# Performance work log

Measured on AMD Instinct MI355X. Metric: run time of the kernel, lower is better.

Reference implementation:

```python
import jax, jax.numpy as jnp
import numpy as np

ARITY = 2
DEPTH = 9          # max_depth: full tree has levels 0..DEPTH
H = 512            # hidden_size
V = 512            # vocab_size
B = 64             # batch
S = 64             # source length


def _preorder_perm(arity, depth):
    # map pre-order position -> flat level-order index
    offs = np.cumsum([0] + [arity ** d for d in range(depth + 1)])
    perm = []
    def rec(d, pos):
        perm.append(int(offs[d] + pos))
        if d < depth:
            for c in range(arity):
                rec(d + 1, pos * arity + c)
    rec(0, 0)
    return np.asarray(perm, dtype=np.int32)

PERM = jnp.asarray(_preorder_perm(ARITY, DEPTH))


def setup_inputs() -> dict:
    key = jax.random.key(0)
    ks = jax.random.split(key, 12)
    s = 0.05
    return {
        "root_hiddens": jax.random.normal(ks[0], (B, H), jnp.float32),
        "ann_emb": jax.random.normal(ks[1], (B, H), jnp.float32),
        "encoder_outputs": jax.random.normal(ks[2], (S, B, H), jnp.float32),
        "source_mask": jnp.ones((B, S), dtype=bool),
        # GRUCell params per child: input_size = 2H (attention concat)
        "w_ih": jax.random.normal(ks[3], (ARITY, 3 * H, 2 * H), jnp.float32) * s,
        "w_hh": jax.random.normal(ks[4], (ARITY, 3 * H, H), jnp.float32) * s,
        "b_ih": jax.random.normal(ks[5], (ARITY, 3 * H), jnp.float32) * s,
        "b_hh": jax.random.normal(ks[6], (ARITY, 3 * H), jnp.float32) * s,
        # hidden2vocab: Linear(H,2H) -> Sigmoid -> Linear(2H,V)
        "W1": jax.random.normal(ks[7], (2 * H, H), jnp.float32) * s,
        "b1": jax.random.normal(ks[8], (2 * H,), jnp.float32) * s,
        "W2": jax.random.normal(ks[9], (V, 2 * H), jnp.float32) * s,
        "b2": jax.random.normal(ks[10], (V,), jnp.float32) * s,
    }


def _gru(x, h, wih, whh, bih, bhh):
    # x: [B,n,2H], h: [B,n,H]; PyTorch GRUCell semantics
    gi = jnp.einsum('bni,gi->bng', x, wih) + bih
    gh = jnp.einsum('bnh,gh->bng', h, whh) + bhh
    i_r, i_z, i_n = jnp.split(gi, 3, axis=-1)
    h_r, h_z, h_n = jnp.split(gh, 3, axis=-1)
    r = jax.nn.sigmoid(i_r + h_r)
    z = jax.nn.sigmoid(i_z + h_z)
    n = jnp.tanh(i_n + r * h_n)
    return (1.0 - z) * n + z * h


def _forward(root_hiddens, ann_emb, encoder_outputs, source_mask,
             w_ih, w_hh, b_ih, b_hh, W1, b1, W2, b2):
    b = root_hiddens.shape[0]
    enc = encoder_outputs.transpose(1, 0, 2)        # [B,S,H]
    h = root_hiddens[:, None, :]                    # [B,1,H]
    prods = []
    for d in range(DEPTH + 1):
        # hidden2vocab at every node of this level
        hid = jax.nn.sigmoid(jnp.einsum('bnh,kh->bnk', h, W1) + b1)
        prods.append(jnp.einsum('bnk,vk->bnv', hid, W2) + b2)
        if d < DEPTH:
            # dot-product attention per node over source positions
            scores = jnp.einsum('bnh,bsh->bns', h, enc)
            scores = jnp.where(source_mask[:, None, :], scores, -1e9)
            a = jax.nn.softmax(scores, axis=-1)
            weighted = jnp.einsum('bns,bsh->bnh', a, enc)
            n = h.shape[1]
            x = jnp.concatenate(
                [jnp.broadcast_to(ann_emb[:, None, :], (b, n, H)), weighted],
                axis=-1)                             # [B,n,2H]
            children = [_gru(x, h, w_ih[c], w_hh[c], b_ih[c], b_hh[c])
                        for c in range(ARITY)]
            h = jnp.stack(children, axis=2).reshape(b, n * ARITY, H)
    out = jnp.concatenate(prods, axis=1)            # [B,N,V] level-order
    out = out[:, PERM, :]                           # pre-order, as torch yields
    return out.transpose(1, 0, 2)                   # [N,B,V] like pad_sequence


def reference(root_hiddens, ann_emb, encoder_outputs, source_mask,
              w_ih, w_hh, b_ih, b_hh, W1, b1, W2, b2):
    return _forward(root_hiddens, ann_emb, encoder_outputs, source_mask,
                    w_ih, w_hh, b_ih, b_hh, W1, b1, W2, b2)
```

## Files before the change

### kernel.cpp

```cpp
#include <hip/hip_runtime.h>


#define BATCH 64
#define HDIM  512

typedef float  floatx4 __attribute__((ext_vector_type(4)));
typedef float  f32x16  __attribute__((ext_vector_type(16)));
typedef short  short8  __attribute__((ext_vector_type(8)));

__device__ __forceinline__ float bf2f(unsigned short u) {
  union { unsigned int i; float f; } v; v.i = ((unsigned int)u) << 16; return v.f;
}
__device__ __forceinline__ unsigned short f2bf(float f) {
  union { float f; unsigned int i; } v; v.f = f;
  unsigned int x = v.i;
  return (unsigned short)((x + 0x7fffu + ((x >> 16) & 1u)) >> 16);
}
__device__ __forceinline__ float sigm(float x) { return 1.f / (1.f + __expf(-x)); }

__device__ __forceinline__ int preorder_idx(int d, int node) {
  int p = 0;
  for (int i = 1; i <= d; ++i) {
    int bit = (node >> (d - i)) & 1;
    p += 1 + bit * ((1 << (10 - i)) - 1);
  }
  return p;
}

__device__ __forceinline__ void gload_lds16(const void* g, void* l) {
  __builtin_amdgcn_global_load_lds(
      (const __attribute__((address_space(1))) unsigned int*)g,
      (__attribute__((address_space(3))) unsigned int*)l, 16, 0, 0);
}

__device__ __forceinline__ void stage_f32(unsigned short* ldst, const float* src) {
  float4 v0 = *(const float4*)src;
  float4 v1 = *(const float4*)(src + 4);
  union { unsigned short s[8]; float4 v; } u;
  u.s[0]=f2bf(v0.x); u.s[1]=f2bf(v0.y); u.s[2]=f2bf(v0.z); u.s[3]=f2bf(v0.w);
  u.s[4]=f2bf(v1.x); u.s[5]=f2bf(v1.y); u.s[6]=f2bf(v1.z); u.s[7]=f2bf(v1.w);
  *(float4*)ldst = u.v;
}

__device__ __forceinline__ void stage_split(unsigned short* dh, unsigned short* dl,
                                            const float* src) {
  float4 v0 = *(const float4*)src;
  float4 v1 = *(const float4*)(src + 4);
  float v[8] = {v0.x, v0.y, v0.z, v0.w, v1.x, v1.y, v1.z, v1.w};
  union { unsigned short s[8]; float4 q; } H, L;
  #pragma unroll
  for (int i = 0; i < 8; ++i) {
    unsigned short hb = f2bf(v[i]);
    H.s[i] = hb;
    L.s[i] = f2bf(v[i] - bf2f(hb));
  }
  *(float4*)dh = H.q;
  *(float4*)dl = L.q;
}

__global__ __launch_bounds__(256) void k_root(const float* __restrict__ root,
                                              float* __restrict__ h0,
                                              unsigned short* __restrict__ bh,
                                              unsigned short* __restrict__ bl) {
  int i = blockIdx.x * 256 + threadIdx.x;
  float v = root[i];
  h0[i] = v;
  int row = i >> 9, k = i & 511;
  int mt = row >> 5, r = row & 31, ktg = k >> 4, oct = (k >> 3) & 1, e = k & 7;
  size_t fo = ((size_t)(mt * 32 + ktg) * 64 + oct * 32 + r) * 8 + e;
  unsigned short hb = f2bf(v);
  bh[fo] = hb;
  bl[fo] = f2bf(v - bf2f(hb));
}

__global__ __launch_bounds__(256) void k_prep_wih(const float* __restrict__ wih,
                                                  unsigned short* __restrict__ dh,
                                                  unsigned short* __restrict__ dl) {
  int idx = blockIdx.x * 256 + threadIdx.x;
  int jr  = idx & 31;
  int oct = (idx >> 5) & 1;
  int ktg = (idx >> 6) & 31;
  int jt  = (idx >> 11) & 15;
  int cg  = idx >> 15;
  int c = cg / 3, g = cg % 3;
  int j = jt * 32 + jr, k = ktg * 16 + oct * 8;
  const float* src = wih + ((size_t)c * 1536 + g * 512 + j) * 1024 + 512 + k;
  float v[8];
  *(float4*)&v[0] = *(const float4*)src;
  *(float4*)&v[4] = *(const float4*)(src + 4);
  union { unsigned short s[8]; float4 q; } H, L;
  #pragma unroll
  for (int i = 0; i < 8; ++i) {
    unsigned short hb = f2bf(v[i]); H.s[i] = hb; L.s[i] = f2bf(v[i] - bf2f(hb));
  }
  *(float4*)(dh + (size_t)idx * 8) = H.q;
  *(float4*)(dl + (size_t)idx * 8) = L.q;
}

__global__ __launch_bounds__(256) void k_prep_whh(const float* __restrict__ whh,
                                                  unsigned short* __restrict__ dh,
                                                  unsigned short* __restrict__ dl) {
  int idx = blockIdx.x * 256 + threadIdx.x;
  int jr  = idx & 31;
  int oct = (idx >> 5) & 1;
  int ktg = (idx >> 6) & 31;
  int jt  = (idx >> 11) & 15;
  int cg  = idx >> 15;
  int c = cg / 3, g = cg % 3;
  int j = jt * 32 + jr, k = ktg * 16 + oct * 8;
  const float* src = whh + ((size_t)c * 1536 + g * 512 + j) * 512 + k;
  float v[8];
  *(float4*)&v[0] = *(const float4*)src;
  *(float4*)&v[4] = *(const float4*)(src + 4);
  union { unsigned short s[8]; float4 q; } H, L;
  #pragma unroll
  for (int i = 0; i < 8; ++i) {
    unsigned short hb = f2bf(v[i]); H.s[i] = hb; L.s[i] = f2bf(v[i] - bf2f(hb));
  }
  *(float4*)(dh + (size_t)idx * 8) = H.q;
  *(float4*)(dl + (size_t)idx * 8) = L.q;
}

__global__ __launch_bounds__(256) void k_prep_encB(const float* __restrict__ enc,
                                                   unsigned short* __restrict__ dh,
                                                   unsigned short* __restrict__ dl) {
  int idx = blockIdx.x * 256 + threadIdx.x;
  int jr  = idx & 31;
  int oct = (idx >> 5) & 1;
  int ktg = (idx >> 6) & 31;
  int jt  = (idx >> 11) & 1;
  int b   = idx >> 12;
  int s = jt * 32 + jr, k = ktg * 16 + oct * 8;
  const float* src = enc + ((size_t)s * 64 + b) * 512 + k;
  float v[8];
  *(float4*)&v[0] = *(const float4*)src;
  *(float4*)&v[4] = *(const float4*)(src + 4);
  union { unsigned short s_[8]; float4 q; } H, L;
  #pragma unroll
  for (int i = 0; i < 8; ++i) {
    unsigned short hb = f2bf(v[i]); H.s_[i] = hb; L.s_[i] = f2bf(v[i] - bf2f(hb));
  }
  *(float4*)(dh + (size_t)idx * 8) = H.q;
  *(float4*)(dl + (size_t)idx * 8) = L.q;
}

__global__ __launch_bounds__(256) void k_prep_encT(const float* __restrict__ enc,
                                                   unsigned short* __restrict__ dh,
                                                   unsigned short* __restrict__ dl) {
  int idx = blockIdx.x * 256 + threadIdx.x;
  int jr  = idx & 31;
  int oct = (idx >> 5) & 1;
  int ktg = (idx >> 6) & 3;
  int jt  = (idx >> 8) & 15;
  int b   = idx >> 12;
  int hcol = jt * 32 + jr, s0 = ktg * 16 + oct * 8;
  float v[8];
  #pragma unroll
  for (int e = 0; e < 8; ++e)
    v[e] = enc[((size_t)(s0 + e) * 64 + b) * 512 + hcol];
  union { unsigned short s_[8]; float4 q; } H, L;
  #pragma unroll
  for (int i = 0; i < 8; ++i) {
    unsigned short hb = f2bf(v[i]); H.s_[i] = hb; L.s_[i] = f2bf(v[i] - bf2f(hb));
  }
  *(float4*)(dh + (size_t)idx * 8) = H.q;
  *(float4*)(dl + (size_t)idx * 8) = L.q;
}

__global__ __launch_bounds__(256) void k_prep_bf(const float* __restrict__ src,
                                                 unsigned short* __restrict__ db) {
  size_t i = ((size_t)blockIdx.x * 256 + threadIdx.x) * 8;
  stage_f32(db + i, src + i);
}

__global__ __launch_bounds__(256) void k_giann(const float* __restrict__ ann,
                                               const float* __restrict__ wih,
                                               float* __restrict__ giann) {
  __shared__ __align__(16) unsigned short lah[64*40], lal[64*40];
  __shared__ __align__(16) unsigned short lwh[64*40], lwl[64*40];
  int t = threadIdx.x, lane = t & 63, wv = t >> 6;
  int jbase = blockIdx.y * 64, c = blockIdx.z;
  const float* wih_c = wih + (size_t)c * 1536 * 1024;
  floatx4 acc[4];
  #pragma unroll
  for (int i = 0; i < 4; ++i) acc[i] = (floatx4)(0.f);
  int srow = t >> 2, skk = (t & 3) * 8;
  for (int k0 = 0; k0 < 512; k0 += 32) {
    stage_split(lah + srow*40 + skk, lal + srow*40 + skk,
                ann + (size_t)srow * 512 + k0 + skk);
    stage_split(lwh + srow*40 + skk, lwl + srow*40 + skk,
                wih_c + (size_t)(jbase + srow) * 1024 + k0 + skk);
    __syncthreads();
    int arow = wv * 16 + (lane & 15), kq = (lane >> 4) * 8;
    short8 ah = *(const short8*)(lah + arow*40 + kq);
    short8 al = *(const short8*)(lal + arow*40 + kq);
    #pragma unroll
    for (int nt = 0; nt < 4; ++nt) {
      int wo = (nt * 16 + (lane & 15)) * 40 + kq;
      short8 wh = *(const short8*)(lwh + wo);
      short8 wl = *(const short8*)(lwl + wo);
      acc[nt] = __builtin_amdgcn_mfma_f32_16x16x32_bf16(ah, wh, acc[nt], 0, 0, 0);
      acc[nt] = __builtin_amdgcn_mfma_f32_16x16x32_bf16(ah, wl, acc[nt], 0, 0, 0);
      acc[nt] = __builtin_amdgcn_mfma_f32_16x16x32_bf16(al, wh, acc[nt], 0, 0, 0);
    }
    __syncthreads();
  }
  int quad = lane >> 4, cl = lane & 15;
  #pragma unroll
  for (int nt = 0; nt < 4; ++nt) {
    int g = jbase + nt * 16 + cl;
    #pragma unroll
    for (int r = 0; r < 4; ++r) {
      int b = wv * 16 + quad * 4 + r;
      giann[((size_t)c * 64 + b) * 1536 + g] = acc[nt][r];
    }
  }
}

__global__ __launch_bounds__(256) void k_attn(const float* __restrict__ h,
                                              const float* __restrict__ enc,
                                              unsigned short* __restrict__ wgh,
                                              unsigned short* __restrict__ wgl,
                                              int d) {
  int lane = threadIdx.x & 63, wv = threadIdx.x >> 6;
  int m = blockIdx.x * 4 + wv;
  int b = m >> d;
  __shared__ __align__(16) float sh[4][512];
  {
    const float4* src = (const float4*)(h + (size_t)m * HDIM);
    float4* dst = (float4*)sh[wv];
    dst[lane] = src[lane];
    dst[lane + 64] = src[lane + 64];
  }
  __syncthreads();
  const float* hr = sh[wv];
  const float* er = enc + ((size_t)lane * BATCH + b) * HDIM;
  float sc = 0.f;
  for (int k = 0; k < HDIM; k += 8) {
    float4 w0 = *(const float4*)(er + k);
    float4 w1 = *(const float4*)(er + k + 4);
    sc += hr[k+0]*w0.x + hr[k+1]*w0.y + hr[k+2]*w0.z + hr[k+3]*w0.w;
    sc += hr[k+4]*w1.x + hr[k+5]*w1.y + hr[k+6]*w1.z + hr[k+7]*w1.w;
  }
  float mx = sc;
  #pragma unroll
  for (int off = 32; off; off >>= 1) mx = fmaxf(mx, __shfl_xor(mx, off));
  float e = __expf(sc - mx);
  float sum = e;
  #pragma unroll
  for (int off = 32; off; off >>= 1) sum += __shfl_xor(sum, off);
  float a = e / sum;
  float acc[8];
  #pragma unroll
  for (int i = 0; i < 8; ++i) acc[i] = 0.f;
  for (int s = 0; s < 64; ++s) {
    float as = __shfl(a, s);
    const float* ep = enc + ((size_t)s * BATCH + b) * HDIM + lane * 8;
    float4 w0 = *(const float4*)ep;
    float4 w1 = *(const float4*)(ep + 4);
    acc[0] += as * w0.x; acc[1] += as * w0.y; acc[2] += as * w0.z; acc[3] += as * w0.w;
    acc[4] += as * w1.x; acc[5] += as * w1.y; acc[6] += as * w1.z; acc[7] += as * w1.w;
  }
  union { unsigned short s[8]; float4 q; } H, L;
  #pragma unroll
  for (int i = 0; i < 8; ++i) {
    unsigned short hb = f2bf(acc[i]); H.s[i] = hb; L.s[i] = f2bf(acc[i] - bf2f(hb));
  }
  int mt = m >> 5, rr = m & 31;
  size_t fo = ((size_t)(mt * 32 + (lane >> 1)) * 64 + (lane & 1) * 32 + rr) * 8;
  *(float4*)(wgh + fo) = H.q;
  *(float4*)(wgl + fo) = L.q;
}

#define MF32(a, b, c) __builtin_amdgcn_mfma_f32_32x32x16_bf16(a, b, c, 0, 0, 0)

__global__ __launch_bounds__(256, 1) void k_attn_mfma(
    const unsigned short* __restrict__ hbh, const unsigned short* __restrict__ hbl,
    const unsigned short* __restrict__ encBh, const unsigned short* __restrict__ encBl,
    const unsigned short* __restrict__ encTh, const unsigned short* __restrict__ encTl,
    unsigned short* __restrict__ wgh, unsigned short* __restrict__ wgl, int d) {
  __shared__ __align__(16) float Sf[4608];
  __shared__ __align__(16) unsigned short PAh[4096], PAl[4096];
  int t = threadIdx.x, lane = t & 63, wv = t >> 6;
  int mbase = blockIdx.x * 64;
  int b = mbase >> d;
  int mtg0 = mbase >> 5;
  {
    int mt = wv >> 1, sh2 = wv & 1;
    f32x16 acc = (f32x16)(0.f);
    size_t ab = ((size_t)(mtg0 + mt) * 32) * 512;
    size_t bb = ((size_t)(b * 2 + sh2) * 32) * 512;
    #pragma unroll 4
    for (int kt = 0; kt < 32; ++kt) {
      size_t o = ((size_t)kt * 64 + lane) * 8;
      short8 ah = *(const short8*)(hbh + ab + o);
      short8 al = *(const short8*)(hbl + ab + o);
      short8 bh = *(const short8*)(encBh + bb + o);
      short8 bl = *(const short8*)(encBl + bb + o);
      acc = MF32(ah, bh, acc);
      acc = MF32(ah, bl, acc);
      acc = MF32(al, bh, acc);
    }
    int col = sh2 * 32 + (lane & 31);
    int rb = mt * 32 + 4 * (lane >> 5);
    #pragma unroll
    for (int r = 0; r < 16; ++r)
      Sf[(rb + (r & 3) + 8 * (r >> 2)) * 68 + col] = acc[r];
  }
  __syncthreads();
  {
    int row = t >> 2, q = t & 3;
    float v[16];
    const float* Sr = Sf + row * 68 + q * 16;
    *(float4*)&v[0]  = *(const float4*)(Sr);
    *(float4*)&v[4]  = *(const float4*)(Sr + 4);
    *(float4*)&v[8]  = *(const float4*)(Sr + 8);
    *(float4*)&v[12] = *(const float4*)(Sr + 12);
    float mx = v[0];
    #pragma unroll
    for (int i = 1; i < 16; ++i) mx = fmaxf(mx, v[i]);
    mx = fmaxf(mx, __shfl_xor(mx, 1));
    mx = fmaxf(mx, __shfl_xor(mx, 2));
    float sum = 0.f;
    #pragma unroll
    for (int i = 0; i < 16; ++i) { v[i] = __expf(v[i] - mx); sum += v[i]; }
    sum += __shfl_xor(sum, 1);
    sum += __shfl_xor(sum, 2);
    float inv = 1.f / sum;
    int wbase = ((row >> 5) * 4 + q) * 64;
    #pragma unroll
    for (int oct = 0; oct < 2; ++oct) {
      union { unsigned short s_[8]; float4 q4; } H, L;
      #pragma unroll
      for (int e = 0; e < 8; ++e) {
        float a = v[oct * 8 + e] * inv;
        unsigned short hb = f2bf(a);
        H.s_[e] = hb; L.s_[e] = f2bf(a - bf2f(hb));
      }
      int w = (wbase + oct * 32 + (row & 31)) * 8;
      *(float4*)(PAh + w) = H.q4;
      *(float4*)(PAl + w) = L.q4;
    }
  }
  __syncthreads();
  f32x16 o2[2][4];
  #pragma unroll
  for (int mt = 0; mt < 2; ++mt)
    #pragma unroll
    for (int jl = 0; jl < 4; ++jl) o2[mt][jl] = (f32x16)(0.f);
  #pragma unroll
  for (int ktg = 0; ktg < 4; ++ktg) {
    short8 pah[2], pal[2];
    #pragma unroll
    for (int mt = 0; mt < 2; ++mt) {
      pah[mt] = *(const short8*)(PAh + ((mt * 4 + ktg) * 64 + lane) * 8);
      pal[mt] = *(const short8*)(PAl + ((mt * 4 + ktg) * 64 + lane) * 8);
    }
    #pragma unroll
    for (int jl = 0; jl < 4; ++jl) {
      int jt = wv * 4 + jl;
      size_t eb = (((size_t)(b * 16 + jt) * 4 + ktg) * 64 + lane) * 8;
      short8 ebh = *(const short8*)(encTh + eb);
      short8 ebl = *(const short8*)(encTl + eb);
      #pragma unroll
      for (int mt = 0; mt < 2; ++mt) {
        o2[mt][jl] = MF32(pah[mt], ebh, o2[mt][jl]);
        o2[mt][jl] = MF32(pah[mt], ebl, o2[mt][jl]);
        o2[mt][jl] = MF32(pal[mt], ebh, o2[mt][jl]);
      }
    }
  }
  float* scr = Sf + wv * 1152;
  int jrr = lane & 31, oct = lane >> 5;
  #pragma unroll
  for (int mt = 0; mt < 2; ++mt) {
    #pragma unroll
    for (int jl = 0; jl < 4; ++jl) {
      int col = lane & 31;
      int rb = 4 * (lane >> 5);
      #pragma unroll
      for (int r = 0; r < 16; ++r)
        scr[(rb + (r & 3) + 8 * (r >> 2)) * 36 + col] = o2[mt][jl][r];
      asm volatile("s_waitcnt lgkmcnt(0)" ::: "memory");
      __builtin_amdgcn_sched_barrier(0);
      int jt = wv * 4 + jl;
      #pragma unroll
      for (int kh = 0; kh < 2; ++kh) {
        float vv[8];
        const float* sp = scr + jrr * 36 + kh * 16 + oct * 8;
        *(float4*)&vv[0] = *(const float4*)sp;
        *(float4*)&vv[4] = *(const float4*)(sp + 4);
        union { unsigned short s_[8]; float4 q4; } H, L;
        #pragma unroll
        for (int e = 0; e < 8; ++e) {
          unsigned short hb = f2bf(vv[e]);
          H.s_[e] = hb; L.s_[e] = f2bf(vv[e] - bf2f(hb));
        }
        size_t wo = (((size_t)(mtg0 + mt) * 32 + (jt * 2 + kh)) * 64 + lane) * 8;
        *(float4*)(wgh + wo) = H.q4;
        *(float4*)(wgl + wo) = L.q4;
      }
      asm volatile("s_waitcnt lgkmcnt(0)" ::: "memory");
    }
  }
}

__global__ __launch_bounds__(256) void k_hid(const float* __restrict__ h,
                                             const unsigned short* __restrict__ W1b,
                                             const float* __restrict__ b1,
                                             unsigned short* __restrict__ hid) {
  __shared__ __align__(16) unsigned short la[64 * 40];
  __shared__ __align__(16) unsigned short lw[4][64 * 40];
  int t = threadIdx.x, lane = t & 63, wv = t >> 6;
  int mbase = blockIdx.x * 64, jbase = blockIdx.y * 256;
  floatx4 acc[4][4];
  #pragma unroll
  for (int jt = 0; jt < 4; ++jt)
    #pragma unroll
    for (int i = 0; i < 4; ++i) acc[jt][i] = (floatx4)(0.f);
  int srow = t >> 2, skk = (t & 3) * 8;
  for (int k0 = 0; k0 < 512; k0 += 32) {
    stage_f32(la + srow * 40 + skk, h + (size_t)(mbase + srow) * 512 + k0 + skk);
    #pragma unroll
    for (int jt = 0; jt < 4; ++jt)
      *(float4*)(lw[jt] + srow * 40 + skk) =
          *(const float4*)(W1b + (size_t)(jbase + jt * 64 + srow) * 512 + k0 + skk);
    __syncthreads();
    int arow = wv * 16 + (lane & 15);
    int kq = (lane >> 4) * 8;
    short8 af = *(const short8*)(la + arow * 40 + kq);
    #pragma unroll
    for (int jt = 0; jt < 4; ++jt)
      #pragma unroll
      for (int nt = 0; nt < 4; ++nt) {
        short8 wf = *(const short8*)(lw[jt] + (nt * 16 + (lane & 15)) * 40 + kq);
        acc[jt][nt] = __builtin_amdgcn_mfma_f32_16x16x32_bf16(af, wf, acc[jt][nt], 0, 0, 0);
      }
    __syncthreads();
  }
  int quad = lane >> 4, cl = lane & 15;
  #pragma unroll
  for (int jt = 0; jt < 4; ++jt)
    #pragma unroll
    for (int nt = 0; nt < 4; ++nt) {
      int j = jbase + jt * 64 + nt * 16 + cl;
      float bias = b1[j];
      #pragma unroll
      for (int r = 0; r < 4; ++r) {
        int m = mbase + wv * 16 + quad * 4 + r;
        hid[(size_t)m * 1024 + j] = f2bf(sigm(acc[jt][nt][r] + bias));
      }
    }
}

__global__ __launch_bounds__(256) void k_out(const unsigned short* __restrict__ hid,
                                             const unsigned short* __restrict__ W2b,
                                             const float* __restrict__ b2,
                                             float* __restrict__ out, int d) {
  __shared__ __align__(16) unsigned short la[64 * 40];
  __shared__ __align__(16) unsigned short lw[4][64 * 40];
  int t = threadIdx.x, lane = t & 63, wv = t >> 6;
  int mbase = blockIdx.x * 64, jbase = blockIdx.y * 256;
  floatx4 acc[4][4];
  #pragma unroll
  for (int jt = 0; jt < 4; ++jt)
    #pragma unroll
    for (int i = 0; i < 4; ++i) acc[jt][i] = (floatx4)(0.f);
  int srow = t >> 2, skk = (t & 3) * 8;
  for (int k0 = 0; k0 < 1024; k0 += 32) {
    *(float4*)(la + srow * 40 + skk) =
        *(const float4*)(hid + (size_t)(mbase + srow) * 1024 + k0 + skk);
    #pragma unroll
    for (int jt = 0; jt < 4; ++jt)
      *(float4*)(lw[jt] + srow * 40 + skk) =
          *(const float4*)(W2b + (size_t)(jbase + jt * 64 + srow) * 1024 + k0 + skk);
    __syncthreads();
    int arow = wv * 16 + (lane & 15);
    int kq = (lane >> 4) * 8;
    short8 af = *(const short8*)(la + arow * 40 + kq);
    #pragma unroll
    for (int jt = 0; jt < 4; ++jt)
      #pragma unroll
      for (int nt = 0; nt < 4; ++nt) {
        short8 wf = *(const short8*)(lw[jt] + (nt * 16 + (lane & 15)) * 40 + kq);
        acc[jt][nt] = __builtin_amdgcn_mfma_f32_16x16x32_bf16(af, wf, acc[jt][nt], 0, 0, 0);
      }
    __syncthreads();
  }
  int quad = lane >> 4, cl = lane & 15;
  int nmask = (1 << d) - 1;
  int pv[4], bv[4];
  #pragma unroll
  for (int r = 0; r < 4; ++r) {
    int m = mbase + wv * 16 + quad * 4 + r;
    bv[r] = m >> d;
    pv[r] = preorder_idx(d, m & nmask);
  }
  #pragma unroll
  for (int jt = 0; jt < 4; ++jt)
    #pragma unroll
    for (int nt = 0; nt < 4; ++nt) {
      int j = jbase + jt * 64 + nt * 16 + cl;
      float bias = b2[j];
      #pragma unroll
      for (int r = 0; r < 4; ++r) {
        out[((size_t)pv[r] * BATCH + bv[r]) * 512 + j] = acc[jt][nt][r] + bias;
      }
    }
}

__global__ __launch_bounds__(256, 2) void k_gru(const float* __restrict__ h,
                                             const unsigned short* __restrict__ wgh,
                                             const unsigned short* __restrict__ wgl,
                                             const unsigned short* __restrict__ hbh,
                                             const unsigned short* __restrict__ hbl,
                                             const unsigned short* __restrict__ wihh,
                                             const unsigned short* __restrict__ wihl,
                                             const unsigned short* __restrict__ whhh,
                                             const unsigned short* __restrict__ whhl,
                                             const float* __restrict__ bih,
                                             const float* __restrict__ bhh,
                                             const float* __restrict__ giann,
                                             float* __restrict__ hnext,
                                             unsigned short* __restrict__ nbh,
                                             unsigned short* __restrict__ nbl,
                                             int d, int M, int emit_bf) {
  __shared__ __align__(16) unsigned short smem[3][20 * 512];
  int t = threadIdx.x, lane = t & 63, wv = t >> 6;
  int wm = wv >> 1, wj = wv & 1;
  int c = blockIdx.z;
  int mbase = blockIdx.x * 128, jbase = blockIdx.y * 64;
  int jt0 = jbase >> 5;
  int mb32 = mbase >> 5;
  int mtcap = (M >> 5) - 1;

  f32x16 a_r[2], a_z[2], a_n[2], a_h[2];
  #pragma unroll
  for (int i = 0; i < 2; ++i) {
    a_r[i] = (f32x16)(0.f); a_z[i] = (f32x16)(0.f);
    a_n[i] = (f32x16)(0.f); a_h[i] = (f32x16)(0.f);
  }

  auto stage = [&](int it2, int buf2) {
    int pht = it2 >> 5, kt = it2 & 31;
    const unsigned short* Ah = pht ? hbh : wgh;
    const unsigned short* Al = pht ? hbl : wgl;
    const unsigned short* Wh = pht ? whhh : wihh;
    const unsigned short* Wl = pht ? whhl : wihl;
    #pragma unroll
    for (int q = 0; q < 5; ++q) {
      int f = wv * 5 + q;
      const unsigned short* src;
      if (f < 8) {
        int mtl = f >> 1;
        int mt = mb32 + mtl; if (mt > mtcap) mt = mtcap;
        const unsigned short* blob = (f & 1) ? Al : Ah;
        src = blob + ((size_t)(mt * 32 + kt) * 64 + lane) * 8;
      } else {
        int u = f - 8;
        int g = u >> 2, jtl = (u >> 1) & 1;
        const unsigned short* blob = (u & 1) ? Wl : Wh;
        src = blob + ((size_t)(((c * 3 + g) * 16 + jt0 + jtl) * 32 + kt) * 64
                      + lane) * 8;
      }
      gload_lds16(src, &smem[buf2][f * 512]);
    }
  };

  stage(0, 0);
  stage(1, 1);
  asm volatile("s_waitcnt vmcnt(5)" ::: "memory");
  __builtin_amdgcn_s_barrier();
  __builtin_amdgcn_sched_barrier(0);

  int buf = 0;
  #pragma unroll
  for (int ph = 0; ph < 2; ++ph) {
    f32x16* axr = ph ? a_h : a_n;
    for (int i2 = 0; i2 < 32; ++i2) {
      int it = ph * 32 + i2;
      if (it + 2 < 64) {
        int b2 = buf + 2; if (b2 > 2) b2 -= 3;
        stage(it + 2, b2);
      }
      const unsigned short* bb = smem[buf];
      short8 ah[2], al[2];
      #pragma unroll
      for (int mt = 0; mt < 2; ++mt) {
        int s = (wm * 2 + mt) * 2;
        ah[mt] = *(const short8*)(bb + s * 512 + lane * 8);
        al[mt] = *(const short8*)(bb + (s + 1) * 512 + lane * 8);
      }
      short8 w[3][2];
      #pragma unroll
      for (int g = 0; g < 3; ++g) {
        int s = 8 + (g * 2 + wj) * 2;
        w[g][0] = *(const short8*)(bb + s * 512 + lane * 8);
        w[g][1] = *(const short8*)(bb + (s + 1) * 512 + lane * 8);
      }
      __builtin_amdgcn_s_setprio(1);
      #pragma unroll
      for (int mt = 0; mt < 2; ++mt) {
        short8 AH = ah[mt], AL = al[mt];
        a_r[mt] = MF32(AH, w[0][0], a_r[mt]);
        a_r[mt] = MF32(AH, w[0][1], a_r[mt]);
        a_r[mt] = MF32(AL, w[0][0], a_r[mt]);
        a_z[mt] = MF32(AH, w[1][0], a_z[mt]);
        a_z[mt] = MF32(AH, w[1][1], a_z[mt]);
        a_z[mt] = MF32(AL, w[1][0], a_z[mt]);
        axr[mt] = MF32(AH, w[2][0], axr[mt]);
        axr[mt] = MF32(AH, w[2][1], axr[mt]);
        axr[mt] = MF32(AL, w[2][0], axr[mt]);
      }
      __builtin_amdgcn_s_setprio(0);
      asm volatile("s_waitcnt lgkmcnt(0)" ::: "memory");
      __builtin_amdgcn_sched_barrier(0);
      if (it < 62) {
        asm volatile("s_waitcnt vmcnt(5)" ::: "memory");
      } else if (it == 62) {
        asm volatile("s_waitcnt vmcnt(0)" ::: "memory");
      }
      __builtin_amdgcn_sched_barrier(0);
      __builtin_amdgcn_s_barrier();
      __builtin_amdgcn_sched_barrier(0);
      buf = (buf == 2) ? 0 : buf + 1;
    }
  }

  unsigned short (*trh)[72] = (unsigned short(*)[72])(&smem[0][0]);
  unsigned short (*trl)[72] = (unsigned short(*)[72])(&smem[0][0] + 128 * 72);
  int cl = lane & 31;
  int j = jbase + wj * 32 + cl;
  float br  = bih[c * 1536 + j]        + bhh[c * 1536 + j];
  float bz  = bih[c * 1536 + 512 + j]  + bhh[c * 1536 + 512 + j];
  float bin = bih[c * 1536 + 1024 + j];
  float bhn = bhh[c * 1536 + 1024 + j];
  int rowoff = 4 * (lane >> 5);
  #pragma unroll
  for (int mt = 0; mt < 2; ++mt) {
    int mb0 = mbase + wm * 64 + mt * 32 + rowoff;
    #pragma unroll
    for (int r = 0; r < 16; ++r) {
      int m = mb0 + (r & 3) + 8 * (r >> 2);
      if (m < M) {
        int b = m >> d;
        const float* gp = giann + ((size_t)c * 64 + b) * 1536 + j;
        float rg = sigm(a_r[mt][r] + gp[0] + br);
        float zg = sigm(a_z[mt][r] + gp[512] + bz);
        float ng = tanhf(a_n[mt][r] + gp[1024] + bin + rg * (a_h[mt][r] + bhn));
        float hv = h[(size_t)m * 512 + j];
        float nh = (1.f - zg) * ng + zg * hv;
        hnext[(size_t)(2 * m + c) * 512 + j] = nh;
        if (emit_bf) {
          unsigned short hb = f2bf(nh);
          trh[m - mbase][j - jbase] = hb;
          trl[m - mbase][j - jbase] = f2bf(nh - bf2f(hb));
        }
      }
    }
  }
  if (emit_bf) {
    __syncthreads();
    int a = t >> 7;
    int row = t & 127;
    if (mbase + row < M) {
      const unsigned short* trp = a ? &trl[row][0] : &trh[row][0];
      unsigned short* dst = a ? nbl : nbh;
      int mp = 2 * (mbase + row) + c;
      int mtp = mp >> 5, rp = mp & 31;
      #pragma unroll
      for (int q = 0; q < 8; ++q) {
        int k = jbase + q * 8;
        int ktg = k >> 4, oct = (k >> 3) & 1;
        float4 v = *(const float4*)(trp + q * 8);
        *(float4*)(dst + ((size_t)(mtp * 32 + ktg) * 64 + oct * 32 + rp) * 8) = v;
      }
    }
  }
}

extern "C" void kernel_launch(void* const* d_in, const int* in_sizes, int n_in,
                              void* d_out, int out_size, void* d_ws, size_t ws_size,
                              hipStream_t stream) {
  const float* root = (const float*)d_in[0];
  const float* ann  = (const float*)d_in[1];
  const float* enc  = (const float*)d_in[2];
  const float* wih  = (const float*)d_in[4];
  const float* whh  = (const float*)d_in[5];
  const float* bih  = (const float*)d_in[6];
  const float* bhh  = (const float*)d_in[7];
  const float* W1   = (const float*)d_in[8];
  const float* b1   = (const float*)d_in[9];
  const float* W2   = (const float*)d_in[10];
  const float* b2   = (const float*)d_in[11];
  float* out = (float*)d_out;

  char* ws = (char*)d_ws;
  float* hA = (float*)ws;
  float* hB = (float*)(ws + (size_t)67108864);
  unsigned short* hid  = (unsigned short*)(ws + (size_t)100663296);
  unsigned short* wgh  = (unsigned short*)(ws + (size_t)134217728);
  unsigned short* wgl  = (unsigned short*)(ws + (size_t)150994944);
  unsigned short* hbEh = (unsigned short*)(ws + (size_t)167772160);
  unsigned short* hbEl = (unsigned short*)(ws + (size_t)184549376);
  unsigned short* hbOh = (unsigned short*)(ws + (size_t)201326592);
  unsigned short* hbOl = (unsigned short*)(ws + (size_t)209715200);
  float* giann         = (float*)(ws + (size_t)218103808);
  unsigned short* wihh = (unsigned short*)(ws + (size_t)218890240);
  unsigned short* wihl = (unsigned short*)(ws + (size_t)222035968);
  unsigned short* whhh = (unsigned short*)(ws + (size_t)225181696);
  unsigned short* whhl = (unsigned short*)(ws + (size_t)228327424);
  unsigned short* W1b  = (unsigned short*)(ws + (size_t)231473152);
  unsigned short* W2b  = (unsigned short*)(ws + (size_t)232521728);
  unsigned short* encBh = (unsigned short*)(ws + (size_t)234881024);
  unsigned short* encBl = (unsigned short*)(ws + (size_t)239075328);
  unsigned short* encTh = (unsigned short*)(ws + (size_t)243269632);
  unsigned short* encTl = (unsigned short*)(ws + (size_t)247463936);
  int use_mfma_attn = (ws_size >= (size_t)251658240) ? 1 : 0;

  k_root<<<dim3(128), dim3(256), 0, stream>>>(root, hB, hbEh, hbEl);
  k_prep_wih<<<dim3(768), dim3(256), 0, stream>>>(wih, wihh, wihl);
  k_prep_whh<<<dim3(768), dim3(256), 0, stream>>>(whh, whhh, whhl);
  k_prep_bf<<<dim3(256), dim3(256), 0, stream>>>(W1, W1b);
  k_prep_bf<<<dim3(256), dim3(256), 0, stream>>>(W2, W2b);
  if (use_mfma_attn) {
    k_prep_encB<<<dim3(1024), dim3(256), 0, stream>>>(enc, encBh, encBl);
    k_prep_encT<<<dim3(1024), dim3(256), 0, stream>>>(enc, encTh, encTl);
  }
  k_giann<<<dim3(1, 24, 2), dim3(256), 0, stream>>>(ann, wih, giann);

  float* hcur = hB;
  float* hnxt = hA;
  unsigned short *bhc = hbEh, *blc = hbEl, *bhn = hbOh, *bln = hbOl;
  for (int d = 0; d <= 9; ++d) {
    int n = 1 << d;
    int M = 64 * n;
    k_hid<<<dim3(M / 64, 4), dim3(256), 0, stream>>>(hcur, W1b, b1, hid);
    k_out<<<dim3(M / 64, 2), dim3(256), 0, stream>>>(hid, W2b, b2, out, d);
    if (d < 9) {
      if (use_mfma_attn && d >= 6) {
        k_attn_mfma<<<dim3(M / 64), dim3(256), 0, stream>>>(
            bhc, blc, encBh, encBl, encTh, encTl, wgh, wgl, d);
      } else {
        k_attn<<<dim3(M / 4), dim3(256), 0, stream>>>(hcur, enc, wgh, wgl, d);
      }
      k_gru<<<dim3((M + 127) / 128, 8, 2), dim3(256), 0, stream>>>(
          hcur, wgh, wgl, bhc, blc, wihh, wihl, whhh, whhl, bih, bhh, giann,
          hnxt, bhn, bln, d, M, d < 8 ? 1 : 0);
      float* tmp = hcur; hcur = hnxt; hnxt = tmp;
      unsigned short* ts;
      ts = bhc; bhc = bhn; bhn = ts;
      ts = blc; blc = bln; bln = ts;
    }
  }
}
```

Before: 2.015 ms.

## Stage two k-tiles per barrier and load low weight halves directly to registers

Restructures the k_gru main loop to stage two k-tiles per iteration into a 4-slot LDS ring, halving the number of block barriers and wait points. The low bf16 halves of the weights are no longer staged through LDS; each wave reads its own slice straight from global memory into registers. This shrinks the per-tile LDS footprint and cross-wave synchronisation. In exchange it adds global-load latency inside the compute loop and uses a stricter vmcnt(0) wait every pair, which may reduce overlap.

```diff
diff --git a/kernel.cpp b/kernel.cpp
--- a/kernel.cpp
+++ b/kernel.cpp
@@ -525,7 +525,7 @@
                                              unsigned short* __restrict__ nbh,
                                              unsigned short* __restrict__ nbl,
                                              int d, int M, int emit_bf) {
-  __shared__ __align__(16) unsigned short smem[3][20 * 512];
+  __shared__ __align__(16) unsigned short smem[4][14 * 512];
   int t = threadIdx.x, lane = t & 63, wv = t >> 6;
   int wm = wv >> 1, wj = wv & 1;
   int c = blockIdx.z;
@@ -541,49 +541,54 @@
     a_n[i] = (f32x16)(0.f); a_h[i] = (f32x16)(0.f);
   }
 
-  auto stage = [&](int it2, int buf2) {
-    int pht = it2 >> 5, kt = it2 & 31;
-    const unsigned short* Ah = pht ? hbh : wgh;
-    const unsigned short* Al = pht ? hbl : wgl;
-    const unsigned short* Wh = pht ? whhh : wihh;
-    const unsigned short* Wl = pht ? whhl : wihl;
-    #pragma unroll
-    for (int q = 0; q < 5; ++q) {
-      int f = wv * 5 + q;
+  auto stage_pair = [&](int ktA, int ktB) {
+    #pragma unroll
+    for (int q = 0; q < 7; ++q) {
+      int f = wv * 7 + q;
+      int kt2  = (f < 14) ? ktA : ktB;
+      int slot = (f < 14) ? f : f - 14;
+      int pht = kt2 >> 5, kt = kt2 & 31;
       const unsigned short* src;
-      if (f < 8) {
-        int mtl = f >> 1;
+      if (slot < 8) {
+        int mtl = slot >> 1;
         int mt = mb32 + mtl; if (mt > mtcap) mt = mtcap;
-        const unsigned short* blob = (f & 1) ? Al : Ah;
+        const unsigned short* blob = (slot & 1) ? (pht ? hbl : wgl)
+                                                : (pht ? hbh : wgh);
         src = blob + ((size_t)(mt * 32 + kt) * 64 + lane) * 8;
       } else {
-        int u = f - 8;
-        int g = u >> 2, jtl = (u >> 1) & 1;
-        const unsigned short* blob = (u & 1) ? Wl : Wh;
-        src = blob + ((size_t)(((c * 3 + g) * 16 + jt0 + jtl) * 32 + kt) * 64
-                      + lane) * 8;
-      }
-      gload_lds16(src, &smem[buf2][f * 512]);
+        int u = slot - 8;
+        int g = u >> 1, jtl = u & 1;
+        const unsigned short* Wh = pht ? whhh : wihh;
+        src = Wh + ((size_t)(((c * 3 + g) * 16 + jt0 + jtl) * 32 + kt) * 64
+                    + lane) * 8;
+      }
+      gload_lds16(src, &smem[kt2 & 3][slot * 512]);
     }
   };
 
-  stage(0, 0);
-  stage(1, 1);
-  asm volatile("s_waitcnt vmcnt(5)" ::: "memory");
+  stage_pair(0, 1);
+  asm volatile("s_waitcnt vmcnt(0)" ::: "memory");
   __builtin_amdgcn_s_barrier();
   __builtin_amdgcn_sched_barrier(0);
 
-  int buf = 0;
-  #pragma unroll
-  for (int ph = 0; ph < 2; ++ph) {
+  for (int w = 0; w < 32; ++w) {
+    int ph = w >> 4;
     f32x16* axr = ph ? a_h : a_n;
-    for (int i2 = 0; i2 < 32; ++i2) {
-      int it = ph * 32 + i2;
-      if (it + 2 < 64) {
-        int b2 = buf + 2; if (b2 > 2) b2 -= 3;
-        stage(it + 2, b2);
-      }
-      const unsigned short* bb = smem[buf];
+    const unsigned short* Wl = ph ? whhl : wihl;
+    if (w < 31) stage_pair(2 * w + 2, 2 * w + 3);
+    #pragma unroll
+    for (int e = 0; e < 2; ++e) {
+      int kt2 = 2 * w + e;
+      const unsigned short* bb = smem[kt2 & 3];
+      short8 wlf[3];
+      {
+        int ktm = kt2 & 31;
+        #pragma unroll
+        for (int g = 0; g < 3; ++g)
+          wlf[g] = *(const short8*)(Wl +
+              ((size_t)(((c * 3 + g) * 16 + jt0 + wj) * 32 + ktm) * 64
+               + lane) * 8);
+      }
       short8 ah[2], al[2];
       #pragma unroll
       for (int mt = 0; mt < 2; ++mt) {
@@ -591,40 +596,38 @@
         ah[mt] = *(const short8*)(bb + s * 512 + lane * 8);
         al[mt] = *(const short8*)(bb + (s + 1) * 512 + lane * 8);
       }
-      short8 w[3][2];
-      #pragma unroll
-      for (int g = 0; g < 3; ++g) {
-        int s = 8 + (g * 2 + wj) * 2;
-        w[g][0] = *(const short8*)(bb + s * 512 + lane * 8);
-        w[g][1] = *(const short8*)(bb + (s + 1) * 512 + lane * 8);
-      }
+      short8 whf[3];
+      #pragma unroll
+      for (int g = 0; g < 3; ++g)
+        whf[g] = *(const short8*)(bb + (8 + g * 2 + wj) * 512 + lane * 8);
       __builtin_amdgcn_s_setprio(1);
       #pragma unroll
       for (int mt = 0; mt < 2; ++mt) {
         short8 AH = ah[mt], AL = al[mt];
-        a_r[mt] = MF32(AH, w[0][0], a_r[mt]);
-        a_r[mt] = MF32(AH, w[0][1], a_r[mt]);
-        a_r[mt] = MF32(AL, w[0][0], a_r[mt]);
-        a_z[mt] = MF32(AH, w[1][0], a_z[mt]);
-        a_z[mt] = MF32(AH, w[1][1], a_z[mt]);
-        a_z[mt] = MF32(AL, w[1][0], a_z[mt]);
-        axr[mt] = MF32(AH, w[2][0], axr[mt]);
-        axr[mt] = MF32(AH, w[2][1], axr[mt]);
-        axr[mt] = MF32(AL, w[2][0], axr[mt]);
+        a_r[mt] = MF32(AH, whf[0], a_r[mt]);
+        a_r[mt] = MF32(AL, whf[0], a_r[mt]);
+        a_z[mt] = MF32(AH, whf[1], a_z[mt]);
+        a_z[mt] = MF32(AL, whf[1], a_z[mt]);
+        axr[mt] = MF32(AH, whf[2], axr[mt]);
+        axr[mt] = MF32(AL, whf[2], axr[mt]);
+      }
+      #pragma unroll
+      for (int mt = 0; mt < 2; ++mt) {
+        short8 AH = ah[mt];
+        a_r[mt] = MF32(AH, wlf[0], a_r[mt]);
+        a_z[mt] = MF32(AH, wlf[1], a_z[mt]);
+        axr[mt] = MF32(AH, wlf[2], axr[mt]);
       }
       __builtin_amdgcn_s_setprio(0);
-      asm volatile("s_waitcnt lgkmcnt(0)" ::: "memory");
+    }
+    asm volatile("s_waitcnt lgkmcnt(0)" ::: "memory");
+    __builtin_amdgcn_sched_barrier(0);
+    if (w < 31) {
+      asm volatile("s_waitcnt vmcnt(0)" ::: "memory");
       __builtin_amdgcn_sched_barrier(0);
-      if (it < 62) {
-        asm volatile("s_waitcnt vmcnt(5)" ::: "memory");
-      } else if (it == 62) {
-        asm volatile("s_waitcnt vmcnt(0)" ::: "memory");
-      }
-      __builtin_amdgcn_sched_barrier(0);
-      __builtin_amdgcn_s_barrier();
-      __builtin_amdgcn_sched_barrier(0);
-      buf = (buf == 2) ? 0 : buf + 1;
-    }
+    }
+    __builtin_amdgcn_s_barrier();
+    __builtin_amdgcn_sched_barrier(0);
   }
 
   unsigned short (*trh)[72] = (unsigned short(*)[72])(&smem[0][0]);
```

New measurement: 3.648 ms. 81.1% more time.
